# Kernel tuning notes

Measured on AMD Instinct MI355X. Metric: run time of the kernel, lower is better.

## Reference

```python
import jax, jax.numpy as jnp
import numpy as np

IN_DIM, INTER_DIM, OUT_DIM = 512, 256, 512


def setup_inputs() -> dict:
    key = jax.random.key(0)
    k1, k2, k3, k4 = jax.random.split(key, 4)
    feat_map = jax.random.normal(k1, (8, IN_DIM, 64, 64), dtype=jnp.float32)
    # xavier-uniform-style init scales
    lim_p = float(np.sqrt(6.0 / (IN_DIM + INTER_DIM)))
    lim_w = float(np.sqrt(6.0 / (IN_DIM + OUT_DIM)))
    phi_w = jax.random.uniform(k2, (INTER_DIM, IN_DIM), jnp.float32, -lim_p, lim_p)
    theta_w = jax.random.uniform(k3, (INTER_DIM, IN_DIM), jnp.float32, -lim_p, lim_p)
    weight = jax.random.uniform(k4, (IN_DIM, OUT_DIM), jnp.float32, -lim_w, lim_w)
    return {"feat_map": feat_map, "phi_w": phi_w, "theta_w": theta_w, "weight": weight}


def reference(feat_map, phi_w, theta_w, weight):
    B, D, H, W = feat_map.shape
    # b c h w -> b (h w) c
    feat_vec = jnp.transpose(feat_map.reshape(B, D, H * W), (0, 2, 1))  # [B, HW, D]
    phi = jnp.einsum('bnc,ic->bni', feat_vec, phi_w)      # [B, HW, inter]
    theta = jnp.einsum('bnc,ic->bni', feat_vec, theta_w)  # [B, HW, inter]
    product = jnp.einsum('bni,bmi->bnm', phi, theta)      # [B, HW, HW]
    phi_norm = jnp.linalg.norm(phi, axis=-1, keepdims=True)      # [B, HW, 1]
    theta_norm = jnp.linalg.norm(theta, axis=-1, keepdims=True)  # [B, HW, 1]
    norms = phi_norm * jnp.transpose(theta_norm, (0, 2, 1))      # [B, HW, HW]
    sim = jax.nn.softmax(product / norms, axis=-1)
    out = jnp.einsum('bnm,bmc->bnc', sim, feat_vec)  # [B, HW, D]
    out = jnp.einsum('bnc,cd->bnd', out, weight)     # [B, HW, out_dim]
    # b (h w) d -> b d h w
    updated = jnp.transpose(out, (0, 2, 1)).reshape(B, -1, H, W)
    return jax.nn.relu(updated)
```

## Files before the change

kernel.cpp:

```cpp
#include <hip/hip_runtime.h>


typedef short s8v __attribute__((ext_vector_type(8)));
typedef float f4v __attribute__((ext_vector_type(4)));

__device__ inline ushort f2bf(float x) {
  union { float f; unsigned u; } v; v.f = x;
  unsigned u = v.u + 0x7fff + ((v.u >> 16) & 1);
  return (ushort)(u >> 16);
}

__global__ __launch_bounds__(256) void k0a(const float* __restrict__ feat,
                                           ushort* __restrict__ featT,
                                           ushort* __restrict__ featV) {
  int bid = blockIdx.x;
  int b = bid >> 9, cb = (bid >> 6) & 7, mt = bid & 63;
  int t = threadIdx.x;
  __shared__ ushort tile[64][72];

#pragma unroll
  for (int p = 0; p < 4; p++) {
    int ci = p * 16 + (t >> 4);
    int mi = (t & 15) * 4;
    float4 v = *(const float4*)&feat[((size_t)(b * 512 + cb * 64 + ci)) * 4096 + mt * 64 + mi];
    ushort4 u; u.x = f2bf(v.x); u.y = f2bf(v.y); u.z = f2bf(v.z); u.w = f2bf(v.w);
    *(ushort4*)&featV[((size_t)(b * 64 + mt) * 512 + cb * 64 + ci) * 64 + mi] = u;
    tile[ci][mi] = u.x; tile[ci][mi + 1] = u.y; tile[ci][mi + 2] = u.z; tile[ci][mi + 3] = u.w;
  }
  __syncthreads();
  int m = t >> 2, cs = (t & 3) * 16;
  ushort tmp[16];
#pragma unroll
  for (int j = 0; j < 16; j++) tmp[j] = tile[cs + j][m];
  ushort* dst = &featT[((size_t)(b * 4096 + mt * 64 + m)) * 512 + cb * 64 + cs];
  *(s8v*)dst = *(s8v*)&tmp[0];
  *(s8v*)(dst + 8) = *(s8v*)&tmp[8];
}

__global__ __launch_bounds__(256) void k0b(const float* __restrict__ pw,
                                           const float* __restrict__ tw,
                                           ushort* __restrict__ wbp,
                                           ushort* __restrict__ wbt) {
  int bid = blockIdx.x;
  const float* src = (bid < 128) ? pw : tw;
  ushort* dst = (bid < 128) ? wbp : wbt;
  int idx = ((bid & 127) * 256 + threadIdx.x) * 4;
  float4 v = *(const float4*)&src[idx];
  ushort4 u; u.x = f2bf(v.x); u.y = f2bf(v.y); u.z = f2bf(v.z); u.w = f2bf(v.w);
  *(ushort4*)&dst[idx] = u;
}

__global__ __launch_bounds__(256) void k0c(const float* __restrict__ w,
                                           ushort* __restrict__ wT) {
  int bid = blockIdx.x;
  int cb = bid >> 3, db = bid & 7;
  int t = threadIdx.x;
  __shared__ ushort tile[64][72];
#pragma unroll
  for (int p = 0; p < 4; p++) {
    int ci = p * 16 + (t >> 4);
    int di = (t & 15) * 4;
    float4 v = *(const float4*)&w[(size_t)(cb * 64 + ci) * 512 + db * 64 + di];
    tile[ci][di] = f2bf(v.x); tile[ci][di + 1] = f2bf(v.y);
    tile[ci][di + 2] = f2bf(v.z); tile[ci][di + 3] = f2bf(v.w);
  }
  __syncthreads();
  int d = t >> 2, cs = (t & 3) * 16;
  ushort tmp[16];
#pragma unroll
  for (int j = 0; j < 16; j++) tmp[j] = tile[cs + j][d];
  ushort* dst = &wT[(size_t)(db * 64 + d) * 512 + cb * 64 + cs];
  *(s8v*)dst = *(s8v*)&tmp[0];
  *(s8v*)(dst + 8) = *(s8v*)&tmp[8];
}

__global__ __launch_bounds__(512) void k1_gemm(
    const ushort* __restrict__ featT, const ushort* __restrict__ wbp,
    const ushort* __restrict__ wbt, ushort* __restrict__ phi_n,
    ushort* __restrict__ theta_n) {
  int bid = blockIdx.x;
  int b = bid & 7;
  int rest = bid >> 3;
  int half = rest & 1;
  int nt = rest >> 1;
  const ushort* wb = half ? wbt : wbp;
  ushort* dst = half ? theta_n : phi_n;
  int t = threadIdx.x;
  int lane = t & 63, w = t >> 6;
  int col = lane & 15, quad = lane >> 4;
  int n0 = nt * 128;

  const ushort* abase =
      featT + ((size_t)(b * 4096 + n0 + w * 16 + col)) * 512 + quad * 8;

  f4v acc[16];
#pragma unroll
  for (int i = 0; i < 16; i++) acc[i] = (f4v){0.f, 0.f, 0.f, 0.f};

#pragma unroll 2
  for (int kc = 0; kc < 16; kc++) {
    s8v a = *(const s8v*)(abase + kc * 32);
#pragma unroll
    for (int it = 0; it < 16; it++) {
      s8v bf = *(const s8v*)(wb + (size_t)(it * 16 + col) * 512 + kc * 32 + quad * 8);
      acc[it] = __builtin_amdgcn_mfma_f32_16x16x32_bf16(a, bf, acc[it], 0, 0, 0);
    }
  }
  float rinv[4];
#pragma unroll
  for (int reg = 0; reg < 4; reg++) {
    float ss = 0.f;
#pragma unroll
    for (int it = 0; it < 16; it++) ss += acc[it][reg] * acc[it][reg];
    ss += __shfl_xor(ss, 1); ss += __shfl_xor(ss, 2);
    ss += __shfl_xor(ss, 4); ss += __shfl_xor(ss, 8);
    rinv[reg] = rsqrtf(ss);
  }
#pragma unroll
  for (int it = 0; it < 16; it++) {
#pragma unroll
    for (int reg = 0; reg < 4; reg++) {
      dst[((size_t)(b * 4096 + n0 + w * 16 + quad * 4 + reg)) * 256 + it * 16 + col] =
          f2bf(acc[it][reg] * rinv[reg]);
    }
  }
}

__global__ __launch_bounds__(512) void k3_attn(
    const ushort* __restrict__ phi_n, const ushort* __restrict__ theta_n,
    const ushort* __restrict__ featV, ushort* __restrict__ out1) {
  int bid = blockIdx.x;
  int b = bid & 7;
  int n0 = (bid >> 3) << 6;
  int t = threadIdx.x;
  int lane = t & 63, w = t >> 6;
  int col = lane & 15, quad = lane >> 4;
  int rg = w & 3, mh = w >> 2;
  int l32 = lane & 31, h32 = lane >> 5;

  __shared__ __align__(16) ushort ks[2 * 16384];
  __shared__ __align__(16) ushort ps[4096];
  __shared__ float dred[128];

  s8v qf[8];
  {
    const ushort* qb = phi_n + ((size_t)(b * 4096 + n0 + rg * 16 + col)) * 256 + quad * 8;
#pragma unroll
    for (int f = 0; f < 8; f++) qf[f] = *(const s8v*)(qb + f * 32);
  }

  const ushort* thb = theta_n + (size_t)b * 4096 * 256;
  const ushort* vbb = featV + (size_t)b * 64 * 512 * 64 + (size_t)(w * 64) * 64;

  f4v acc[16];
#pragma unroll
  for (int i = 0; i < 16; i++) acc[i] = (f4v){0.f, 0.f, 0.f, 0.f};
  float denp[4] = {0.f, 0.f, 0.f, 0.f};

#pragma unroll
  for (int u = 0; u < 4; u++) {
    int row = w * 8 + u * 2 + h32;
    s8v val = *(const s8v*)(thb + (size_t)row * 256 + l32 * 8);
    *(s8v*)(ks + row * 256 + ((l32 ^ (row & 7)) * 8)) = val;
  }
  __syncthreads();

#pragma unroll 1
  for (int mt = 0; mt < 64; mt++) {
    const ushort* kc_ = ks + (mt & 1) * 16384;
    ushort* kn_ = ks + ((mt & 1) ^ 1) * 16384;

    s8v kreg[4];
    if (mt < 63) {
      int m1 = (mt + 1) << 6;
#pragma unroll
      for (int u = 0; u < 4; u++) {
        int row = w * 8 + u * 2 + h32;
        kreg[u] = *(const s8v*)(thb + (size_t)(m1 + row) * 256 + l32 * 8);
      }
    }
    s8v v0[4], v1[4];
    {
      const ushort* vb = vbb + (size_t)mt * 32768;
#pragma unroll
      for (int ct = 0; ct < 4; ct++) {
        const ushort* p = vb + (ct * 16 + col) * 64 + quad * 8;
        v0[ct] = *(const s8v*)p;
        v1[ct] = *(const s8v*)(p + 32);
      }
    }

    f4v sv0 = (f4v){0.f, 0.f, 0.f, 0.f};
    f4v sv1 = (f4v){0.f, 0.f, 0.f, 0.f};
    {
      int rm = mh * 32 + col;
      const ushort* kb = kc_ + rm * 256;
#pragma unroll
      for (int kk = 0; kk < 8; kk++) {
        int pos = ((kk * 4 + quad) ^ (col & 7)) * 8;
        s8v b0 = *(const s8v*)(kb + pos);
        s8v b1 = *(const s8v*)(kb + 16 * 256 + pos);
        sv0 = __builtin_amdgcn_mfma_f32_16x16x32_bf16(qf[kk], b0, sv0, 0, 0, 0);
        sv1 = __builtin_amdgcn_mfma_f32_16x16x32_bf16(qf[kk], b1, sv1, 0, 0, 0);
      }
    }
    float p0[4], p1[4];
#pragma unroll
    for (int r = 0; r < 4; r++) {
      p0[r] = __expf(sv0[r]);
      p1[r] = __expf(sv1[r]);
      denp[r] += p0[r] + p1[r];
    }

    __syncthreads();

#pragma unroll
    for (int r = 0; r < 4; r++) {
      int n = rg * 16 + quad * 4 + r;
      int j0 = mh * 4 + (col >> 3);
      ps[n * 64 + ((j0 ^ (n & 7)) * 8) + (col & 7)] = f2bf(p0[r]);
      ps[n * 64 + (((j0 + 2) ^ (n & 7)) * 8) + (col & 7)] = f2bf(p1[r]);
    }
    if (mt < 63) {
#pragma unroll
      for (int u = 0; u < 4; u++) {
        int row = w * 8 + u * 2 + h32;
        *(s8v*)(kn_ + row * 256 + ((l32 ^ (row & 7)) * 8)) = kreg[u];
      }
    }
    __syncthreads();

#pragma unroll
    for (int rs = 0; rs < 4; rs++) {
      const ushort* pb = ps + (rs * 16 + col) * 64;
      s8v pf0 = *(const s8v*)(pb + ((quad ^ (col & 7)) * 8));
      s8v pf1 = *(const s8v*)(pb + (((quad + 4) ^ (col & 7)) * 8));
#pragma unroll
      for (int ct = 0; ct < 4; ct++) {
        acc[rs * 4 + ct] =
            __builtin_amdgcn_mfma_f32_16x16x32_bf16(pf0, v0[ct], acc[rs * 4 + ct], 0, 0, 0);
        acc[rs * 4 + ct] =
            __builtin_amdgcn_mfma_f32_16x16x32_bf16(pf1, v1[ct], acc[rs * 4 + ct], 0, 0, 0);
      }
    }
  }

#pragma unroll
  for (int r = 0; r < 4; r++) {
    float d = denp[r];
    d += __shfl_xor(d, 1); d += __shfl_xor(d, 2);
    d += __shfl_xor(d, 4); d += __shfl_xor(d, 8);
    denp[r] = d;
  }
  if (col == 0) {
#pragma unroll
    for (int r = 0; r < 4; r++) dred[mh * 64 + rg * 16 + quad * 4 + r] = denp[r];
  }
  __syncthreads();
  if (t < 64) dred[t] = 1.0f / (dred[t] + dred[64 + t]);
  __syncthreads();

#pragma unroll
  for (int rs = 0; rs < 4; rs++) {
#pragma unroll
    for (int ct = 0; ct < 4; ct++) {
#pragma unroll
      for (int reg = 0; reg < 4; reg++) {
        int n = rs * 16 + quad * 4 + reg;
        out1[((size_t)(b * 4096 + n0 + n)) * 512 + w * 64 + ct * 16 + col] =
            f2bf(acc[rs * 4 + ct][reg] * dred[n]);
      }
    }
  }
}

__global__ __launch_bounds__(512) void k4_out(
    const ushort* __restrict__ out1, const ushort* __restrict__ wT,
    float* __restrict__ out) {
  int bid = blockIdx.x;
  int b = bid & 7;
  int rest = bid >> 3;
  int dt = rest & 3;
  int nt = rest >> 2;
  int t = threadIdx.x;
  int lane = t & 63, w = t >> 6;
  int col = lane & 15, quad = lane >> 4;
  int dw = w & 1, nw = w >> 1;
  int d0 = dt * 128 + dw * 64;
  int n0 = nt * 256 + nw * 64;

  f4v acc[16];
#pragma unroll
  for (int i = 0; i < 16; i++) acc[i] = (f4v){0.f, 0.f, 0.f, 0.f};

#pragma unroll 2
  for (int kc = 0; kc < 16; kc++) {
    s8v af[4], bf[4];
#pragma unroll
    for (int rs = 0; rs < 4; rs++)
      af[rs] = *(const s8v*)(wT + (size_t)(d0 + rs * 16 + col) * 512 + kc * 32 + quad * 8);
#pragma unroll
    for (int ct = 0; ct < 4; ct++)
      bf[ct] = *(const s8v*)(out1 + ((size_t)(b * 4096 + n0 + ct * 16 + col)) * 512 +
                             kc * 32 + quad * 8);
#pragma unroll
    for (int rs = 0; rs < 4; rs++)
#pragma unroll
      for (int ct = 0; ct < 4; ct++)
        acc[rs * 4 + ct] =
            __builtin_amdgcn_mfma_f32_16x16x32_bf16(af[rs], bf[ct], acc[rs * 4 + ct], 0, 0, 0);
  }
#pragma unroll
  for (int rs = 0; rs < 4; rs++) {
#pragma unroll
    for (int ct = 0; ct < 4; ct++) {
#pragma unroll
      for (int reg = 0; reg < 4; reg++) {
        int d = d0 + rs * 16 + quad * 4 + reg;
        int n = n0 + ct * 16 + col;
        out[((size_t)(b * 512 + d)) * 4096 + n] = fmaxf(acc[rs * 4 + ct][reg], 0.f);
      }
    }
  }
}

extern "C" void kernel_launch(void* const* d_in, const int* in_sizes, int n_in,
                              void* d_out, int out_size, void* d_ws, size_t ws_size,
                              hipStream_t stream) {
  const float* feat    = (const float*)d_in[0];
  const float* phi_w   = (const float*)d_in[1];
  const float* theta_w = (const float*)d_in[2];
  const float* weight  = (const float*)d_in[3];
  float* out = (float*)d_out;

  ushort* wsu = (ushort*)d_ws;
  ushort* featT   = wsu;
  ushort* featV   = wsu + 16777216;
  ushort* phi_n   = wsu + 33554432;
  ushort* theta_n = wsu + 41943040;
  ushort* wbp     = wsu + 50331648;
  ushort* wbt     = wsu + 50462720;
  ushort* weightT = wsu + 50593792;
  ushort* out1    = wsu;

  k0a<<<dim3(4096), dim3(256), 0, stream>>>(feat, featT, featV);
  k0b<<<dim3(256), dim3(256), 0, stream>>>(phi_w, theta_w, wbp, wbt);
  k0c<<<dim3(64), dim3(256), 0, stream>>>(weight, weightT);
  k1_gemm<<<dim3(512), dim3(512), 0, stream>>>(featT, wbp, wbt, phi_n, theta_n);
  k3_attn<<<dim3(512), dim3(512), 0, stream>>>(phi_n, theta_n, featV, out1);
  k4_out<<<dim3(512), dim3(512), 0, stream>>>(out1, weightT, out);
}
```

Baseline: 607.0 us.

## Double-buffer P tile, remap QK warps to share K fragments, add setprio

```diff
diff --git a/kernel.cpp b/kernel.cpp
--- a/kernel.cpp
+++ b/kernel.cpp
@@ -126,7 +126,7 @@
   }
 }
 
-__global__ __launch_bounds__(512) void k3_attn(
+__global__ __launch_bounds__(512, 2) void k3_attn(
     const ushort* __restrict__ phi_n, const ushort* __restrict__ theta_n,
     const ushort* __restrict__ featV, ushort* __restrict__ out1) {
   int bid = blockIdx.x;
@@ -135,18 +135,22 @@
   int t = threadIdx.x;
   int lane = t & 63, w = t >> 6;
   int col = lane & 15, quad = lane >> 4;
-  int rg = w & 3, mh = w >> 2;
+  int mh4 = w & 3, rh = w >> 2;
   int l32 = lane & 31, h32 = lane >> 5;
+  int cs = col & 7;
 
   __shared__ __align__(16) ushort ks[2 * 16384];
-  __shared__ __align__(16) ushort ps[4096];
-  __shared__ float dred[128];
-
-  s8v qf[8];
+  __shared__ __align__(16) ushort ps[2 * 4096];
+  __shared__ float dred[4 * 64];
+
+  s8v qfA[8], qfB[8];
   {
-    const ushort* qb = phi_n + ((size_t)(b * 4096 + n0 + rg * 16 + col)) * 256 + quad * 8;
-#pragma unroll
-    for (int f = 0; f < 8; f++) qf[f] = *(const s8v*)(qb + f * 32);
+    const ushort* qa = phi_n + ((size_t)(b * 4096 + n0 + rh * 32 + col)) * 256 + quad * 8;
+#pragma unroll
+    for (int f = 0; f < 8; f++) qfA[f] = *(const s8v*)(qa + f * 32);
+    const ushort* qb = qa + 16 * 256;
+#pragma unroll
+    for (int f = 0; f < 8; f++) qfB[f] = *(const s8v*)(qb + f * 32);
   }
 
   const ushort* thb = theta_n + (size_t)b * 4096 * 256;
@@ -155,7 +159,7 @@
   f4v acc[16];
 #pragma unroll
   for (int i = 0; i < 16; i++) acc[i] = (f4v){0.f, 0.f, 0.f, 0.f};
-  float denp[4] = {0.f, 0.f, 0.f, 0.f};
+  float denp[8] = {0.f, 0.f, 0.f, 0.f, 0.f, 0.f, 0.f, 0.f};
 
 #pragma unroll
   for (int u = 0; u < 4; u++) {
@@ -169,6 +173,7 @@
   for (int mt = 0; mt < 64; mt++) {
     const ushort* kc_ = ks + (mt & 1) * 16384;
     ushort* kn_ = ks + ((mt & 1) ^ 1) * 16384;
+    ushort* pw_ = ps + (mt & 1) * 4096;
 
     s8v kreg[4];
     if (mt < 63) {
@@ -190,36 +195,39 @@
       }
     }
 
-    f4v sv0 = (f4v){0.f, 0.f, 0.f, 0.f};
-    f4v sv1 = (f4v){0.f, 0.f, 0.f, 0.f};
+    f4v svA = (f4v){0.f, 0.f, 0.f, 0.f};
+    f4v svB = (f4v){0.f, 0.f, 0.f, 0.f};
     {
-      int rm = mh * 32 + col;
-      const ushort* kb = kc_ + rm * 256;
+      const ushort* kb = kc_ + (mh4 * 16 + col) * 256;
+      __builtin_amdgcn_s_setprio(1);
 #pragma unroll
       for (int kk = 0; kk < 8; kk++) {
-        int pos = ((kk * 4 + quad) ^ (col & 7)) * 8;
-        s8v b0 = *(const s8v*)(kb + pos);
-        s8v b1 = *(const s8v*)(kb + 16 * 256 + pos);
-        sv0 = __builtin_amdgcn_mfma_f32_16x16x32_bf16(qf[kk], b0, sv0, 0, 0, 0);
-        sv1 = __builtin_amdgcn_mfma_f32_16x16x32_bf16(qf[kk], b1, sv1, 0, 0, 0);
-      }
-    }
-    float p0[4], p1[4];
+        int pos = ((kk * 4 + quad) ^ cs) * 8;
+        s8v bf = *(const s8v*)(kb + pos);
+        svA = __builtin_amdgcn_mfma_f32_16x16x32_bf16(qfA[kk], bf, svA, 0, 0, 0);
+        svB = __builtin_amdgcn_mfma_f32_16x16x32_bf16(qfB[kk], bf, svB, 0, 0, 0);
+      }
+      __builtin_amdgcn_s_setprio(0);
+    }
+
+    float pA[4], pB[4];
 #pragma unroll
     for (int r = 0; r < 4; r++) {
-      p0[r] = __expf(sv0[r]);
-      p1[r] = __expf(sv1[r]);
-      denp[r] += p0[r] + p1[r];
-    }
-
-    __syncthreads();
-
-#pragma unroll
-    for (int r = 0; r < 4; r++) {
-      int n = rg * 16 + quad * 4 + r;
-      int j0 = mh * 4 + (col >> 3);
-      ps[n * 64 + ((j0 ^ (n & 7)) * 8) + (col & 7)] = f2bf(p0[r]);
-      ps[n * 64 + (((j0 + 2) ^ (n & 7)) * 8) + (col & 7)] = f2bf(p1[r]);
+      pA[r] = __expf(svA[r]);
+      pB[r] = __expf(svB[r]);
+      denp[r] += pA[r];
+      denp[4 + r] += pB[r];
+    }
+
+    {
+      int j0 = mh4 * 2 + (col >> 3);
+#pragma unroll
+      for (int r = 0; r < 4; r++) {
+        int nA = rh * 32 + quad * 4 + r;
+        pw_[nA * 64 + ((j0 ^ (nA & 7)) * 8) + cs] = f2bf(pA[r]);
+        int nB = nA + 16;
+        pw_[nB * 64 + ((j0 ^ (nB & 7)) * 8) + cs] = f2bf(pB[r]);
+      }
     }
     if (mt < 63) {
 #pragma unroll
@@ -230,11 +238,12 @@
     }
     __syncthreads();
 
+    __builtin_amdgcn_s_setprio(1);
 #pragma unroll
     for (int rs = 0; rs < 4; rs++) {
-      const ushort* pb = ps + (rs * 16 + col) * 64;
-      s8v pf0 = *(const s8v*)(pb + ((quad ^ (col & 7)) * 8));
-      s8v pf1 = *(const s8v*)(pb + (((quad + 4) ^ (col & 7)) * 8));
+      const ushort* pb = pw_ + (rs * 16 + col) * 64;
+      s8v pf0 = *(const s8v*)(pb + ((quad ^ cs) * 8));
+      s8v pf1 = *(const s8v*)(pb + (((quad + 4) ^ cs) * 8));
 #pragma unroll
       for (int ct = 0; ct < 4; ct++) {
         acc[rs * 4 + ct] =
@@ -243,21 +252,25 @@
             __builtin_amdgcn_mfma_f32_16x16x32_bf16(pf1, v1[ct], acc[rs * 4 + ct], 0, 0, 0);
       }
     }
-  }
-
-#pragma unroll
-  for (int r = 0; r < 4; r++) {
-    float d = denp[r];
+    __builtin_amdgcn_s_setprio(0);
+  }
+
+#pragma unroll
+  for (int i = 0; i < 8; i++) {
+    float d = denp[i];
     d += __shfl_xor(d, 1); d += __shfl_xor(d, 2);
     d += __shfl_xor(d, 4); d += __shfl_xor(d, 8);
-    denp[r] = d;
+    denp[i] = d;
   }
   if (col == 0) {
 #pragma unroll
-    for (int r = 0; r < 4; r++) dred[mh * 64 + rg * 16 + quad * 4 + r] = denp[r];
-  }
-  __syncthreads();
-  if (t < 64) dred[t] = 1.0f / (dred[t] + dred[64 + t]);
+    for (int i = 0; i < 8; i++) {
+      int n = rh * 32 + (i >> 2) * 16 + quad * 4 + (i & 3);
+      dred[mh4 * 64 + n] = denp[i];
+    }
+  }
+  __syncthreads();
+  if (t < 64) dred[t] = 1.0f / (dred[t] + dred[64 + t] + dred[128 + t] + dred[192 + t]);
   __syncthreads();
 
 #pragma unroll
```

Result: no change. 599.6 us (-1.2%).
